# Performance work log

Measured on AMD Instinct MI355X. Metric: run time of the kernel, lower is better.

Reference implementation:

```python
import jax, jax.numpy as jnp
import numpy as np

EPS_NORM = 1e-12  # F.normalize eps
SINK_EPS = 0.1    # entropic regularization
THRESH = 0.01
MAX_ITERS = 100


def _l2_normalize(x):
    n = jnp.linalg.norm(x, axis=1, keepdims=True)
    return x / jnp.maximum(n, EPS_NORM)


def _sinkhorn(K, u, v):
    # K: [M, N], u: [M], v: [N]. Mirrors the torch loop with early stop on err < thresh.
    def cond(state):
        i, r, c, err = state
        return jnp.logical_and(i < MAX_ITERS, err >= THRESH)

    def body(state):
        i, r, c, _ = state
        r0 = r
        r = u / (K @ c)          # [M]
        c = v / (K.T @ r)        # [N]
        err = jnp.mean(jnp.abs(r - r0))
        return (i + 1, r, c, err)

    init = (jnp.int32(0), jnp.ones_like(u), jnp.ones_like(v), jnp.float32(1e9))
    _, r, c, _ = jax.lax.while_loop(cond, body, init)
    return jnp.outer(r, c) * K   # [M, N]


def _ot(src, tgt):
    # src: [M, D] (gt cluster centers), tgt: [N, D] (local features)
    s = _l2_normalize(src)
    t = _l2_normalize(tgt)
    sim = s @ t.T                         # [M, N], differentiable
    M, N = sim.shape
    u = jnp.full((M,), 1.0 / M, sim.dtype)
    v = jnp.full((N,), 1.0 / N, sim.dtype)
    K = jax.lax.stop_gradient(jnp.exp(-(1.0 - sim) / SINK_EPS))  # no_grad in torch
    T = jax.lax.stop_gradient(_sinkhorn(K, u, v))
    return jnp.sum(T * sim)


def setup_inputs() -> dict:
    key = jax.random.key(0)
    k1, k2, k3, k4 = jax.random.split(key, 4)
    E, B, D = 3, 4096, 1024
    M, N = 5, 256
    return {
        "feature": jax.random.normal(k1, (E, B, D), jnp.float32),
        "gt": jax.random.normal(k2, (E, B, D), jnp.float32),
        "gt_local": jax.random.normal(k3, (E, M, D), jnp.float32),
        "feature_local": jax.random.normal(k4, (E, N, D), jnp.float32),
    }


def reference(feature, gt, gt_local, feature_local):
    E = feature.shape[0]
    # global term: (1/E) * sum_e mean_b sum_d feature*gt
    loss_global = jnp.mean(jnp.sum(feature * gt, axis=-1))
    # local OT term per extractor: OT(gt_local, feature_local) * 2, then / E
    ot_vals = jax.vmap(_ot)(gt_local, feature_local)  # [E]
    loss_local = jnp.sum(ot_vals * 2.0) / E
    return loss_global + loss_local * 0.1
```

## Files before the change

### kernel.cpp

```cpp
#include <hip/hip_runtime.h>
#include <math.h>

typedef float f32x4 __attribute__((ext_vector_type(4)));

#define NSIM_BLOCKS 48
#define NDOT_BLOCKS 2048
#define THREADS 256
#define TOTAL_F4 3145728
#define DOT_STRIDE (NDOT_BLOCKS * THREADS)

__global__ __launch_bounds__(256) void fused_main(
    const f32x4* __restrict__ f4, const f32x4* __restrict__ g4,
    const float* __restrict__ gt_local, const float* __restrict__ feat_local,
    float* __restrict__ ws_partials, float* __restrict__ ws_sim)
{
    __shared__ float s_sh[5120];
    const int tid = threadIdx.x;
    const int lane = tid & 63;
    const int wid = tid >> 6;

    if (blockIdx.x < NDOT_BLOCKS) {
        const int base = blockIdx.x * THREADS + tid;
        const f32x4 a0 = f4[base + 0 * DOT_STRIDE];
        const f32x4 b0 = g4[base + 0 * DOT_STRIDE];
        const f32x4 a1 = f4[base + 1 * DOT_STRIDE];
        const f32x4 b1 = g4[base + 1 * DOT_STRIDE];
        const f32x4 a2 = f4[base + 2 * DOT_STRIDE];
        const f32x4 b2 = g4[base + 2 * DOT_STRIDE];
        const f32x4 a3 = f4[base + 3 * DOT_STRIDE];
        const f32x4 b3 = g4[base + 3 * DOT_STRIDE];
        const f32x4 a4 = f4[base + 4 * DOT_STRIDE];
        const f32x4 b4 = g4[base + 4 * DOT_STRIDE];
        const f32x4 a5 = f4[base + 5 * DOT_STRIDE];
        const f32x4 b5 = g4[base + 5 * DOT_STRIDE];
        f32x4 p0 = a0 * b0 + a1 * b1;
        f32x4 p1 = a2 * b2 + a3 * b3;
        f32x4 p2 = a4 * b4 + a5 * b5;
        f32x4 p = p0 + p1 + p2;
        float acc = p.x + p.y + p.z + p.w;
        #pragma unroll
        for (int o = 32; o; o >>= 1) acc += __shfl_xor(acc, o);
        if (lane == 0) s_sh[wid] = acc;
        __syncthreads();
        if (tid == 0)
            ws_partials[blockIdx.x] = s_sh[0] + s_sh[1] + s_sh[2] + s_sh[3];
    } else {
        const int b = blockIdx.x - NDOT_BLOCKS;
        const int e = b >> 4;
        const int chunk = b & 15;
        const f32x4* sbase = (const f32x4*)(gt_local + e * 5120);
        #pragma unroll
        for (int k = 0; k < 5; ++k)
            ((f32x4*)s_sh)[tid + 256 * k] = sbase[tid + 256 * k];
        __syncthreads();
        for (int m = wid; m < 5; m += 4) {
            float acc = 0.f;
            #pragma unroll
            for (int k = 0; k < 16; ++k) {
                float v = s_sh[m * 1024 + lane + 64 * k];
                acc += v * v;
            }
            #pragma unroll
            for (int o = 32; o; o >>= 1) acc += __shfl_xor(acc, o);
            const float rinv = 1.f / fmaxf(sqrtf(acc), 1e-12f);
            #pragma unroll
            for (int k = 0; k < 16; ++k)
                s_sh[m * 1024 + lane + 64 * k] *= rinv;
        }
        __syncthreads();
        for (int rr = 0; rr < 4; ++rr) {
            const int n = chunk * 16 + wid * 4 + rr;
            const float* trow = feat_local + (e * 256 + n) * 1024;
            float a0 = 0.f, a1 = 0.f, a2 = 0.f, a3 = 0.f, a4 = 0.f, at = 0.f;
            #pragma unroll
            for (int k = 0; k < 16; ++k) {
                const int d = lane + 64 * k;
                const float tv = trow[d];
                at += tv * tv;
                a0 += tv * s_sh[d];
                a1 += tv * s_sh[1024 + d];
                a2 += tv * s_sh[2048 + d];
                a3 += tv * s_sh[3072 + d];
                a4 += tv * s_sh[4096 + d];
            }
            #pragma unroll
            for (int o = 32; o; o >>= 1) {
                at += __shfl_xor(at, o);
                a0 += __shfl_xor(a0, o);
                a1 += __shfl_xor(a1, o);
                a2 += __shfl_xor(a2, o);
                a3 += __shfl_xor(a3, o);
                a4 += __shfl_xor(a4, o);
            }
            if (lane == 0) {
                const float rnt = 1.f / fmaxf(sqrtf(at), 1e-12f);
                float* dst = ws_sim + e * 5 * 256 + n;
                dst[0]    = a0 * rnt;
                dst[256]  = a1 * rnt;
                dst[512]  = a2 * rnt;
                dst[768]  = a3 * rnt;
                dst[1024] = a4 * rnt;
            }
        }
    }
}

__global__ __launch_bounds__(256) void finalize_kernel(
    const float* __restrict__ ws_partials, const float* __restrict__ ws_sim,
    float* __restrict__ out)
{
    __shared__ float ot_sh[3];
    __shared__ double g_sh;
    const int tid = threadIdx.x;
    const int lane = tid & 63;
    const int wid = tid >> 6;

    if (wid < 3) {
        const int e = wid;
        float K[5][4], S[5][4];
        #pragma unroll
        for (int m = 0; m < 5; ++m)
            #pragma unroll
            for (int j = 0; j < 4; ++j) {
                const float s = ws_sim[(e * 5 + m) * 256 + lane + 64 * j];
                S[m][j] = s;
                K[m][j] = expf(-(1.0f - s) / 0.1f);
            }
        float r[5] = {1.f, 1.f, 1.f, 1.f, 1.f};
        float c[4] = {1.f, 1.f, 1.f, 1.f};
        float err;
        int it = 0;
        do {
            float r0[5];
            #pragma unroll
            for (int m = 0; m < 5; ++m) r0[m] = r[m];
            #pragma unroll
            for (int m = 0; m < 5; ++m) {
                float p = K[m][0] * c[0] + K[m][1] * c[1] +
                          K[m][2] * c[2] + K[m][3] * c[3];
                #pragma unroll
                for (int o = 32; o; o >>= 1) p += __shfl_xor(p, o);
                r[m] = 0.2f / p;
            }
            #pragma unroll
            for (int j = 0; j < 4; ++j) {
                const float q = K[0][j] * r[0] + K[1][j] * r[1] +
                                K[2][j] * r[2] + K[3][j] * r[3] +
                                K[4][j] * r[4];
                c[j] = (1.0f / 256.0f) / q;
            }
            err = (fabsf(r[0] - r0[0]) + fabsf(r[1] - r0[1]) +
                   fabsf(r[2] - r0[2]) + fabsf(r[3] - r0[3]) +
                   fabsf(r[4] - r0[4])) * 0.2f;
            ++it;
        } while (it < 100 && err >= 0.01f);

        float ot = 0.f;
        #pragma unroll
        for (int m = 0; m < 5; ++m)
            #pragma unroll
            for (int j = 0; j < 4; ++j)
                ot += r[m] * c[j] * K[m][j] * S[m][j];
        #pragma unroll
        for (int o = 32; o; o >>= 1) ot += __shfl_xor(ot, o);
        if (lane == 0) ot_sh[e] = ot;
    } else {
        double acc = 0.0;
        #pragma unroll
        for (int k = 0; k < 32; ++k) acc += (double)ws_partials[lane + 64 * k];
        #pragma unroll
        for (int o = 32; o; o >>= 1) acc += __shfl_xor(acc, o);
        if (lane == 0) g_sh = acc;
    }
    __syncthreads();
    if (tid == 0) {
        const float loss_global = (float)(g_sh / 12288.0);
        const float loss_local = (ot_sh[0] + ot_sh[1] + ot_sh[2]) * 2.0f / 3.0f;
        out[0] = loss_global + 0.1f * loss_local;
    }
}

extern "C" void kernel_launch(void* const* d_in, const int* in_sizes, int n_in,
                              void* d_out, int out_size, void* d_ws, size_t ws_size,
                              hipStream_t stream) {
    const f32x4* f4 = (const f32x4*)d_in[0];
    const f32x4* g4 = (const f32x4*)d_in[1];
    const float* gt_local = (const float*)d_in[2];
    const float* feat_local = (const float*)d_in[3];
    float* ws_partials = (float*)d_ws;
    float* ws_sim = ws_partials + NDOT_BLOCKS;
    float* out = (float*)d_out;

    hipLaunchKernelGGL(fused_main, dim3(NDOT_BLOCKS + NSIM_BLOCKS), dim3(THREADS),
                       0, stream, f4, g4, gt_local, feat_local, ws_partials, ws_sim);
    hipLaunchKernelGGL(finalize_kernel, dim3(1), dim3(THREADS), 0, stream,
                       ws_partials, ws_sim, out);
}
```

Before: 127.6 us.

## Move Sinkhorn into per-extractor sim blocks overlapping the global dot reduction

Sim computation is consolidated into one block per extractor that keeps the similarity matrix in shared memory and runs the Sinkhorn iterations in-kernel, concurrently with the bandwidth-bound dot-product blocks. The finalize kernel shrinks to a 64-thread reduction of the partials and three OT values. This aims to take the serial Sinkhorn loop off the critical path after the main kernel. In exchange, each sim block does far more serial work (256 rows per block), which could lengthen the tail if it exceeds the dot phase.

```diff
diff --git a/kernel.cpp b/kernel.cpp
--- a/kernel.cpp
+++ b/kernel.cpp
@@ -3,24 +3,30 @@
 
 typedef float f32x4 __attribute__((ext_vector_type(4)));
 
-#define NSIM_BLOCKS 48
+#define NSIM_BLOCKS 3
 #define NDOT_BLOCKS 2048
 #define THREADS 256
 #define TOTAL_F4 3145728
 #define DOT_STRIDE (NDOT_BLOCKS * THREADS)
 
+#define WS_OT_OFF 2048
+
 __global__ __launch_bounds__(256) void fused_main(
     const f32x4* __restrict__ f4, const f32x4* __restrict__ g4,
     const float* __restrict__ gt_local, const float* __restrict__ feat_local,
-    float* __restrict__ ws_partials, float* __restrict__ ws_sim)
+    float* __restrict__ ws)
 {
     __shared__ float s_sh[5120];
+    __shared__ float sim_sh[5][256];
+    float* ws_partials = ws;
+    float* ws_ot = ws + WS_OT_OFF;
+
     const int tid = threadIdx.x;
     const int lane = tid & 63;
     const int wid = tid >> 6;
 
-    if (blockIdx.x < NDOT_BLOCKS) {
-        const int base = blockIdx.x * THREADS + tid;
+    if (blockIdx.x >= NSIM_BLOCKS) {
+        const int base = (blockIdx.x - NSIM_BLOCKS) * THREADS + tid;
         const f32x4 a0 = f4[base + 0 * DOT_STRIDE];
         const f32x4 b0 = g4[base + 0 * DOT_STRIDE];
         const f32x4 a1 = f4[base + 1 * DOT_STRIDE];
@@ -40,142 +46,133 @@
         float acc = p.x + p.y + p.z + p.w;
         #pragma unroll
         for (int o = 32; o; o >>= 1) acc += __shfl_xor(acc, o);
-        if (lane == 0) s_sh[wid] = acc;
+        if (lane == 0) sim_sh[0][wid] = acc;
         __syncthreads();
         if (tid == 0)
-            ws_partials[blockIdx.x] = s_sh[0] + s_sh[1] + s_sh[2] + s_sh[3];
-    } else {
-        const int b = blockIdx.x - NDOT_BLOCKS;
-        const int e = b >> 4;
-        const int chunk = b & 15;
-        const f32x4* sbase = (const f32x4*)(gt_local + e * 5120);
+            ws_partials[blockIdx.x - NSIM_BLOCKS] =
+                sim_sh[0][0] + sim_sh[0][1] + sim_sh[0][2] + sim_sh[0][3];
+        return;
+    }
+
+    const int e = blockIdx.x;
+    const f32x4* sbase = (const f32x4*)(gt_local + e * 5120);
+    #pragma unroll
+    for (int k = 0; k < 5; ++k)
+        ((f32x4*)s_sh)[tid + 256 * k] = sbase[tid + 256 * k];
+    __syncthreads();
+    for (int m = wid; m < 5; m += 4) {
+        float acc = 0.f;
         #pragma unroll
-        for (int k = 0; k < 5; ++k)
-            ((f32x4*)s_sh)[tid + 256 * k] = sbase[tid + 256 * k];
-        __syncthreads();
-        for (int m = wid; m < 5; m += 4) {
-            float acc = 0.f;
-            #pragma unroll
-            for (int k = 0; k < 16; ++k) {
-                float v = s_sh[m * 1024 + lane + 64 * k];
-                acc += v * v;
-            }
-            #pragma unroll
-            for (int o = 32; o; o >>= 1) acc += __shfl_xor(acc, o);
-            const float rinv = 1.f / fmaxf(sqrtf(acc), 1e-12f);
-            #pragma unroll
-            for (int k = 0; k < 16; ++k)
-                s_sh[m * 1024 + lane + 64 * k] *= rinv;
+        for (int k = 0; k < 16; ++k) {
+            float v = s_sh[m * 1024 + lane + 64 * k];
+            acc += v * v;
         }
-        __syncthreads();
-        for (int rr = 0; rr < 4; ++rr) {
-            const int n = chunk * 16 + wid * 4 + rr;
-            const float* trow = feat_local + (e * 256 + n) * 1024;
-            float a0 = 0.f, a1 = 0.f, a2 = 0.f, a3 = 0.f, a4 = 0.f, at = 0.f;
-            #pragma unroll
-            for (int k = 0; k < 16; ++k) {
-                const int d = lane + 64 * k;
-                const float tv = trow[d];
-                at += tv * tv;
-                a0 += tv * s_sh[d];
-                a1 += tv * s_sh[1024 + d];
-                a2 += tv * s_sh[2048 + d];
-                a3 += tv * s_sh[3072 + d];
-                a4 += tv * s_sh[4096 + d];
-            }
-            #pragma unroll
-            for (int o = 32; o; o >>= 1) {
-                at += __shfl_xor(at, o);
-                a0 += __shfl_xor(a0, o);
-                a1 += __shfl_xor(a1, o);
-                a2 += __shfl_xor(a2, o);
-                a3 += __shfl_xor(a3, o);
-                a4 += __shfl_xor(a4, o);
-            }
-            if (lane == 0) {
-                const float rnt = 1.f / fmaxf(sqrtf(at), 1e-12f);
-                float* dst = ws_sim + e * 5 * 256 + n;
-                dst[0]    = a0 * rnt;
-                dst[256]  = a1 * rnt;
-                dst[512]  = a2 * rnt;
-                dst[768]  = a3 * rnt;
-                dst[1024] = a4 * rnt;
-            }
+        #pragma unroll
+        for (int o = 32; o; o >>= 1) acc += __shfl_xor(acc, o);
+        const float rinv = 1.f / fmaxf(sqrtf(acc), 1e-12f);
+        #pragma unroll
+        for (int k = 0; k < 16; ++k)
+            s_sh[m * 1024 + lane + 64 * k] *= rinv;
+    }
+    __syncthreads();
+    for (int i = 0; i < 64; ++i) {
+        const int n = wid * 64 + i;
+        const float* trow = feat_local + (e * 256 + n) * 1024;
+        float a0 = 0.f, a1 = 0.f, a2 = 0.f, a3 = 0.f, a4 = 0.f, at = 0.f;
+        #pragma unroll
+        for (int k = 0; k < 16; ++k) {
+            const int d = lane + 64 * k;
+            const float tv = trow[d];
+            at += tv * tv;
+            a0 += tv * s_sh[d];
+            a1 += tv * s_sh[1024 + d];
+            a2 += tv * s_sh[2048 + d];
+            a3 += tv * s_sh[3072 + d];
+            a4 += tv * s_sh[4096 + d];
+        }
+        #pragma unroll
+        for (int o = 32; o; o >>= 1) {
+            at += __shfl_xor(at, o);
+            a0 += __shfl_xor(a0, o);
+            a1 += __shfl_xor(a1, o);
+            a2 += __shfl_xor(a2, o);
+            a3 += __shfl_xor(a3, o);
+            a4 += __shfl_xor(a4, o);
+        }
+        if (lane == 0) {
+            const float rnt = 1.f / fmaxf(sqrtf(at), 1e-12f);
+            sim_sh[0][n] = a0 * rnt;
+            sim_sh[1][n] = a1 * rnt;
+            sim_sh[2][n] = a2 * rnt;
+            sim_sh[3][n] = a3 * rnt;
+            sim_sh[4][n] = a4 * rnt;
         }
     }
+    __syncthreads();
+    if (wid != 0) return;
+
+    float K[5][4], S[5][4];
+    #pragma unroll
+    for (int m = 0; m < 5; ++m)
+        #pragma unroll
+        for (int j = 0; j < 4; ++j) {
+            const float s = sim_sh[m][lane + 64 * j];
+            S[m][j] = s;
+            K[m][j] = expf(-(1.0f - s) / 0.1f);
+        }
+    float r[5] = {1.f, 1.f, 1.f, 1.f, 1.f};
+    float c[4] = {1.f, 1.f, 1.f, 1.f};
+    float err;
+    int it = 0;
+    do {
+        float r0[5];
+        #pragma unroll
+        for (int m = 0; m < 5; ++m) r0[m] = r[m];
+        #pragma unroll
+        for (int m = 0; m < 5; ++m) {
+            float p = K[m][0] * c[0] + K[m][1] * c[1] +
+                      K[m][2] * c[2] + K[m][3] * c[3];
+            #pragma unroll
+            for (int o = 32; o; o >>= 1) p += __shfl_xor(p, o);
+            r[m] = 0.2f / p;
+        }
+        #pragma unroll
+        for (int j = 0; j < 4; ++j) {
+            const float q = K[0][j] * r[0] + K[1][j] * r[1] +
+                            K[2][j] * r[2] + K[3][j] * r[3] +
+                            K[4][j] * r[4];
+            c[j] = (1.0f / 256.0f) / q;
+        }
+        err = (fabsf(r[0] - r0[0]) + fabsf(r[1] - r0[1]) +
+               fabsf(r[2] - r0[2]) + fabsf(r[3] - r0[3]) +
+               fabsf(r[4] - r0[4])) * 0.2f;
+        ++it;
+    } while (it < 100 && err >= 0.01f);
+
+    float ot = 0.f;
+    #pragma unroll
+    for (int m = 0; m < 5; ++m)
+        #pragma unroll
+        for (int j = 0; j < 4; ++j)
+            ot += r[m] * c[j] * K[m][j] * S[m][j];
+    #pragma unroll
+    for (int o = 32; o; o >>= 1) ot += __shfl_xor(ot, o);
+    if (lane == 0) ws_ot[e] = ot;
 }
 
-__global__ __launch_bounds__(256) void finalize_kernel(
-    const float* __restrict__ ws_partials, const float* __restrict__ ws_sim,
-    float* __restrict__ out)
+__global__ __launch_bounds__(64) void finalize_kernel(
+    const float* __restrict__ ws, float* __restrict__ out)
 {
-    __shared__ float ot_sh[3];
-    __shared__ double g_sh;
-    const int tid = threadIdx.x;
-    const int lane = tid & 63;
-    const int wid = tid >> 6;
-
-    if (wid < 3) {
-        const int e = wid;
-        float K[5][4], S[5][4];
-        #pragma unroll
-        for (int m = 0; m < 5; ++m)
-            #pragma unroll
-            for (int j = 0; j < 4; ++j) {
-                const float s = ws_sim[(e * 5 + m) * 256 + lane + 64 * j];
-                S[m][j] = s;
-                K[m][j] = expf(-(1.0f - s) / 0.1f);
-            }
-        float r[5] = {1.f, 1.f, 1.f, 1.f, 1.f};
-        float c[4] = {1.f, 1.f, 1.f, 1.f};
-        float err;
-        int it = 0;
-        do {
-            float r0[5];
-            #pragma unroll
-            for (int m = 0; m < 5; ++m) r0[m] = r[m];
-            #pragma unroll
-            for (int m = 0; m < 5; ++m) {
-                float p = K[m][0] * c[0] + K[m][1] * c[1] +
-                          K[m][2] * c[2] + K[m][3] * c[3];
-                #pragma unroll
-                for (int o = 32; o; o >>= 1) p += __shfl_xor(p, o);
-                r[m] = 0.2f / p;
-            }
-            #pragma unroll
-            for (int j = 0; j < 4; ++j) {
-                const float q = K[0][j] * r[0] + K[1][j] * r[1] +
-                                K[2][j] * r[2] + K[3][j] * r[3] +
-                                K[4][j] * r[4];
-                c[j] = (1.0f / 256.0f) / q;
-            }
-            err = (fabsf(r[0] - r0[0]) + fabsf(r[1] - r0[1]) +
-                   fabsf(r[2] - r0[2]) + fabsf(r[3] - r0[3]) +
-                   fabsf(r[4] - r0[4])) * 0.2f;
-            ++it;
-        } while (it < 100 && err >= 0.01f);
-
-        float ot = 0.f;
-        #pragma unroll
-        for (int m = 0; m < 5; ++m)
-            #pragma unroll
-            for (int j = 0; j < 4; ++j)
-                ot += r[m] * c[j] * K[m][j] * S[m][j];
-        #pragma unroll
-        for (int o = 32; o; o >>= 1) ot += __shfl_xor(ot, o);
-        if (lane == 0) ot_sh[e] = ot;
-    } else {
-        double acc = 0.0;
-        #pragma unroll
-        for (int k = 0; k < 32; ++k) acc += (double)ws_partials[lane + 64 * k];
-        #pragma unroll
-        for (int o = 32; o; o >>= 1) acc += __shfl_xor(acc, o);
-        if (lane == 0) g_sh = acc;
-    }
-    __syncthreads();
-    if (tid == 0) {
-        const float loss_global = (float)(g_sh / 12288.0);
-        const float loss_local = (ot_sh[0] + ot_sh[1] + ot_sh[2]) * 2.0f / 3.0f;
+    const int lane = threadIdx.x;
+    double acc = 0.0;
+    #pragma unroll
+    for (int k = 0; k < 32; ++k) acc += (double)ws[lane + 64 * k];
+    #pragma unroll
+    for (int o = 32; o; o >>= 1) acc += __shfl_xor(acc, o);
+    if (lane == 0) {
+        const float loss_global = (float)(acc / 12288.0);
+        const float loss_local =
+            (ws[WS_OT_OFF] + ws[WS_OT_OFF + 1] + ws[WS_OT_OFF + 2]) * 2.0f / 3.0f;
         out[0] = loss_global + 0.1f * loss_local;
     }
 }
@@ -187,12 +184,10 @@
     const f32x4* g4 = (const f32x4*)d_in[1];
     const float* gt_local = (const float*)d_in[2];
     const float* feat_local = (const float*)d_in[3];
-    float* ws_partials = (float*)d_ws;
-    float* ws_sim = ws_partials + NDOT_BLOCKS;
+    float* ws = (float*)d_ws;
     float* out = (float*)d_out;
 
-    hipLaunchKernelGGL(fused_main, dim3(NDOT_BLOCKS + NSIM_BLOCKS), dim3(THREADS),
-                       0, stream, f4, g4, gt_local, feat_local, ws_partials, ws_sim);
-    hipLaunchKernelGGL(finalize_kernel, dim3(1), dim3(THREADS), 0, stream,
-                       ws_partials, ws_sim, out);
+    hipLaunchKernelGGL(fused_main, dim3(NSIM_BLOCKS + NDOT_BLOCKS), dim3(THREADS),
+                       0, stream, f4, g4, gt_local, feat_local, ws);
+    hipLaunchKernelGGL(finalize_kernel, dim3(1), dim3(64), 0, stream, ws, out);
 }
```

After: 190.5 us. 1.49x slower.
